# Performance work log

Measured on AMD Instinct MI355X. Metric: run time of the kernel, lower is better.

## Reference

```python
import jax, jax.numpy as jnp
import numpy as np
import math

N, T, D, H = 256, 32, 1024, 1024

def setup_inputs() -> dict:
    key = jax.random.key(0)
    k1, k2, k3, k4, k5 = jax.random.split(key, 5)
    x = jax.random.normal(k1, (N, T, D), dtype=jnp.float32)
    A = jax.random.normal(k2, (N, H, 4, 4), dtype=jnp.float32)
    Wx = jax.random.normal(k3, (D, 4 * H), dtype=jnp.float32) / math.sqrt(D)
    Wh = jax.random.normal(k4, (H, 4 * H), dtype=jnp.float32) / math.sqrt(H)
    Wattn = jax.random.normal(k5, (H, 4 * H), dtype=jnp.float32) / math.sqrt(H)
    b = jnp.zeros((4 * H,), dtype=jnp.float32)
    return {"x": x, "A": A, "Wx": Wx, "Wh": Wh, "Wattn": Wattn, "b": b}

def _forward(x, A, Wx, Wh, Wattn, b):
    Aflat = A.reshape(A.shape[0], A.shape[1], -1)  # (N, H, 16)
    h0 = Aflat.mean(axis=2)  # mean over 4x4 spatial grid -> (N, H)
    c0 = h0
    scale = 1.0 / math.sqrt(Aflat.shape[1])

    def step(carry, xt):
        prev_h, prev_c = carry
        # scaled dot-product attention over 16 spatial locations
        w = jax.nn.softmax(jnp.einsum('nh,nhl->nl', prev_h, Aflat) * scale, axis=-1)  # (N,16)
        attn = jnp.einsum('nhl,nl->nh', Aflat, w)  # (N,H)
        preact = xt @ Wx + prev_h @ Wh + attn @ Wattn + b  # (N,4H)
        ai, af, ao, ag = jnp.split(preact, 4, axis=1)
        i = jax.nn.sigmoid(ai)
        f = jax.nn.sigmoid(af)
        o = jax.nn.sigmoid(ao)
        g = jnp.tanh(ag)
        next_c = f * prev_c + i * g
        next_h = o * jnp.tanh(next_c)
        return (next_h, next_c), next_h

    xT = jnp.swapaxes(x, 0, 1)  # (T, N, D)
    _, hs = jax.lax.scan(step, (h0, c0), xT)
    return jnp.swapaxes(hs, 0, 1)  # (N, T, H)

def reference(x, A, Wx, Wh, Wattn, b):
    return _forward(x, A, Wx, Wh, Wattn, b)
```

## Files before the change

kernel.cpp:

```cpp
#include <hip/hip_runtime.h>

#define N_B 256
#define T_SEQ 32
#define DD 1024
#define HH 1024

typedef short short8 __attribute__((ext_vector_type(8)));
typedef float floatx4 __attribute__((ext_vector_type(4)));
typedef unsigned short ushort_t;

__device__ __align__(16) ushort_t g_Wxt[(size_t)4096 * 1024];
__device__ __align__(16) ushort_t g_W2 [(size_t)4096 * 2048];
__device__ __align__(16) ushort_t g_xb [(size_t)8192 * 1024];
__device__ __align__(16) float    g_px [(size_t)8192 * 4096];
__device__ __align__(16) ushort_t g_Ab [(size_t)N_B * 16384];
__device__ __align__(16) ushort_t g_At [(size_t)N_B * 16384];
__device__ __align__(16) ushort_t g_Hc[2][N_B * 2048];
__device__ __align__(16) float    g_c [N_B * HH];

__device__ __forceinline__ float bf2f(ushort_t u){
    union { unsigned int i; float f; } v; v.i = ((unsigned int)u) << 16; return v.f;
}
__device__ __forceinline__ ushort_t f2bf(float f){
    union { unsigned int i; float f; } v; v.f = f;
    unsigned int i = v.i;
    unsigned int r = (i + 0x7FFFu + ((i >> 16) & 1u)) >> 16;
    return (ushort_t)r;
}
__device__ __forceinline__ void gload16(const ushort_t* g, ushort_t* l) {
    __builtin_amdgcn_global_load_lds((const __attribute__((address_space(1))) void*)g,
                                     (__attribute__((address_space(3))) void*)l, 16, 0, 0);
}
__device__ __forceinline__ void unp8(uint4 u, float* f) {
    const ushort_t* s = (const ushort_t*)&u;
    #pragma unroll
    for (int i = 0; i < 8; ++i) f[i] = bf2f(s[i]);
}

__global__ __launch_bounds__(128) void cvt_x(const float* __restrict__ x)
{
    int b = blockIdx.x;
    int n = b >> 5, tt = b & 31;
    int tid = threadIdx.x;
    const float* src = x + (size_t)b * 1024 + tid * 8;
    float4 a = *(const float4*)src;
    float4 c = *(const float4*)(src + 4);
    ushort_t r[8];
    r[0]=f2bf(a.x); r[1]=f2bf(a.y); r[2]=f2bf(a.z); r[3]=f2bf(a.w);
    r[4]=f2bf(c.x); r[5]=f2bf(c.y); r[6]=f2bf(c.z); r[7]=f2bf(c.w);
    *(uint4*)(g_xb + (size_t)(tt * 256 + n) * 1024 + tid * 8) = *(const uint4*)r;
}

__global__ __launch_bounds__(256) void cvt_a(const float* __restrict__ A)
{
    int n = blockIdx.x, tid = threadIdx.x;
    int h0 = tid * 4;
    const float* ap = A + (size_t)n * 16384;
    ushort_t tmp[4][16];
    #pragma unroll
    for (int i = 0; i < 4; ++i) {
        const float* row = ap + (size_t)(h0 + i) * 16;
        #pragma unroll
        for (int l = 0; l < 16; ++l) tmp[i][l] = f2bf(row[l]);
        ushort_t* dst = g_Ab + (size_t)n * 16384 + (size_t)(h0 + i) * 16;
        *(uint4*)dst       = *(const uint4*)&tmp[i][0];
        *(uint4*)(dst + 8) = *(const uint4*)&tmp[i][8];
    }
    #pragma unroll
    for (int l = 0; l < 16; ++l) {
        ushort_t pk[4] = { tmp[0][l], tmp[1][l], tmp[2][l], tmp[3][l] };
        *(uint2*)(g_At + (size_t)n * 16384 + (size_t)l * 1024 + h0) = *(const uint2*)pk;
    }
}

__global__ __launch_bounds__(256) void prepack_wx(const float* __restrict__ Wx)
{
    __shared__ ushort_t tile[64][66];
    int k0 = blockIdx.x * 64, j0 = blockIdx.y * 64;
    int c = threadIdx.x & 63, r4 = threadIdx.x >> 6;
    for (int rr = 0; rr < 64; rr += 4) {
        int r = rr + r4;
        tile[r][c] = f2bf(Wx[(size_t)(k0 + r) * 4096 + j0 + c]);
    }
    __syncthreads();
    for (int rr = 0; rr < 64; rr += 4) {
        int j = rr + r4;
        g_Wxt[(size_t)(j0 + j) * 1024 + k0 + c] = tile[c][j];
    }
}

__global__ __launch_bounds__(256) void prepack_w2(
    const float* __restrict__ Wh, const float* __restrict__ Wattn)
{
    __shared__ ushort_t tile[64][66];
    int k0 = blockIdx.x * 64, j0 = blockIdx.y * 64;
    const float* src = (k0 < 1024) ? Wh : Wattn;
    int krel = (k0 < 1024) ? k0 : k0 - 1024;
    int c = threadIdx.x & 63, r4 = threadIdx.x >> 6;
    for (int rr = 0; rr < 64; rr += 4) {
        int r = rr + r4;
        tile[r][c] = f2bf(src[(size_t)(krel + r) * 4096 + j0 + c]);
    }
    __syncthreads();
    for (int rr = 0; rr < 64; rr += 4) {
        int j = rr + r4;
        g_W2[(size_t)(j0 + j) * 2048 + k0 + c] = tile[c][j];
    }
}

__global__ __launch_bounds__(256) void init_hc(const float* __restrict__ A)
{
    int gid = blockIdx.x * 256 + threadIdx.x;
    int n = gid >> 10, h = gid & 1023;
    const float* ap = A + ((size_t)gid << 4);
    float4 a0 = *(const float4*)(ap);
    float4 a1 = *(const float4*)(ap + 4);
    float4 a2 = *(const float4*)(ap + 8);
    float4 a3 = *(const float4*)(ap + 12);
    float s = (a0.x+a0.y+a0.z+a0.w) + (a1.x+a1.y+a1.z+a1.w)
            + (a2.x+a2.y+a2.z+a2.w) + (a3.x+a3.y+a3.z+a3.w);
    s *= (1.0f / 16.0f);
    g_Hc[0][n * 2048 + h] = f2bf(s);
    g_c[gid] = s;
}

__global__ __launch_bounds__(256) void xw_gemm(const float* __restrict__ bias)
{
    __shared__ __align__(16) char smem[33280];
    ushort_t* lA = (ushort_t*)smem;
    ushort_t* lB = (ushort_t*)(smem + 16384);
    float*    lP = (float*)smem;

    int b = blockIdx.x;
    int mb = b >> 5, jb = b & 31;
    int m0 = mb * 128, j0 = jb * 128;
    int tid = threadIdx.x, lane = tid & 63, wv = tid >> 6;
    int wm = wv >> 1, wn = wv & 1;
    int lm = lane & 15, quad = lane >> 4;

    int srow = lane >> 3, sseg = lane & 7;
    const ushort_t* gA = g_xb  + (size_t)(m0 + wv * 32 + srow) * 1024 + (sseg ^ srow) * 8;
    const ushort_t* gB = g_Wxt + (size_t)(j0 + wv * 32 + srow) * 1024 + (sseg ^ srow) * 8;

    floatx4 acc[4][4] = {};
    for (int kt = 0; kt < 16; ++kt) {
        __syncthreads();
        #pragma unroll
        for (int i = 0; i < 4; ++i) {
            gload16(gA + (size_t)i * 8 * 1024 + kt * 64, lA + (wv * 32 + i * 8) * 64);
            gload16(gB + (size_t)i * 8 * 1024 + kt * 64, lB + (wv * 32 + i * 8) * 64);
        }
        __syncthreads();
        #pragma unroll
        for (int ks = 0; ks < 2; ++ks) {
            short8 af[4], bf[4];
            #pragma unroll
            for (int i = 0; i < 4; ++i) {
                int row = wm*64 + i*16 + lm;
                af[i] = *(const short8*)(lA + row * 64 + (((ks*4 + quad) ^ (row & 7)) * 8));
            }
            #pragma unroll
            for (int j = 0; j < 4; ++j) {
                int row = wn*64 + j*16 + lm;
                bf[j] = *(const short8*)(lB + row * 64 + (((ks*4 + quad) ^ (row & 7)) * 8));
            }
            #pragma unroll
            for (int i = 0; i < 4; ++i)
                #pragma unroll
                for (int j = 0; j < 4; ++j)
                    acc[i][j] = __builtin_amdgcn_mfma_f32_16x16x32_bf16(af[i], bf[j], acc[i][j], 0, 0, 0);
        }
    }

    #pragma unroll
    for (int ph = 0; ph < 2; ++ph) {
        __syncthreads();
        if (wm == ph) {
            #pragma unroll
            for (int i = 0; i < 4; ++i)
                #pragma unroll
                for (int j = 0; j < 4; ++j)
                    #pragma unroll
                    for (int q = 0; q < 4; ++q)
                        lP[(i*16 + quad*4 + q) * 130 + wn*64 + j*16 + lm] = acc[i][j][q];
        }
        __syncthreads();
        int row = tid >> 2, seg = tid & 3;
        const float* src = lP + row * 130 + seg * 32;
        float* dst = g_px + (size_t)(m0 + ph * 64 + row) * 4096 + j0 + seg * 32;
        const float* bb = bias + j0 + seg * 32;
        #pragma unroll
        for (int i = 0; i < 8; ++i) {
            float4 v = *(const float4*)(src + i * 4);
            float4 w = *(const float4*)(bb + i * 4);
            v.x += w.x; v.y += w.y; v.z += w.z; v.w += w.w;
            *(float4*)(dst + i * 4) = v;
        }
    }
}

__global__ __launch_bounds__(256) void attn_step(int t)
{
    ushort_t* Hc = g_Hc[t & 1];
    int n = blockIdx.x, tid = threadIdx.x;
    int lane = tid & 63, wv = tid >> 6;
    const ushort_t* hp = Hc + n * 2048;

    int hc = lane * 16;
    float hv[16];
    unp8(*(const uint4*)(hp + hc), hv);
    unp8(*(const uint4*)(hp + hc + 8), hv + 8);

    __shared__ float red[16];
    float lg[4];
    #pragma unroll
    for (int l4 = 0; l4 < 4; ++l4) {
        int l = wv * 4 + l4;
        const ushort_t* ar = g_At + (size_t)n * 16384 + (size_t)l * 1024 + hc;
        float av[16];
        unp8(*(const uint4*)ar, av);
        unp8(*(const uint4*)(ar + 8), av + 8);
        float s = 0.f;
        #pragma unroll
        for (int i = 0; i < 16; ++i) s += hv[i] * av[i];
        s += __shfl_xor(s, 32); s += __shfl_xor(s, 16); s += __shfl_xor(s, 8);
        s += __shfl_xor(s, 4);  s += __shfl_xor(s, 2);  s += __shfl_xor(s, 1);
        lg[l4] = s;
    }
    if (lane == 0) {
        #pragma unroll
        for (int l4 = 0; l4 < 4; ++l4) red[wv * 4 + l4] = lg[l4];
    }
    __syncthreads();
    float w[16], mx = -1e30f;
    #pragma unroll
    for (int l = 0; l < 16; ++l) {
        float s = red[l] * 0.03125f;
        w[l] = s; mx = fmaxf(mx, s);
    }
    float sum = 0.f;
    #pragma unroll
    for (int l = 0; l < 16; ++l) { w[l] = __expf(w[l] - mx); sum += w[l]; }
    float inv = 1.f / sum;
    #pragma unroll
    for (int l = 0; l < 16; ++l) w[l] *= inv;

    int h0 = tid * 4;
    const ushort_t* ab = g_Ab + (size_t)n * 16384 + (size_t)h0 * 16;
    ushort_t outp[4];
    #pragma unroll
    for (int i = 0; i < 4; ++i) {
        float av[16];
        unp8(*(const uint4*)(ab + i * 16), av);
        unp8(*(const uint4*)(ab + i * 16 + 8), av + 8);
        float acc = 0.f;
        #pragma unroll
        for (int l = 0; l < 16; ++l) acc += av[l] * w[l];
        outp[i] = f2bf(acc);
    }
    *(uint2*)(Hc + n * 2048 + 1024 + h0) = *(const uint2*)outp;
}

__global__ __launch_bounds__(256, 2) void step_gemm(float* __restrict__ out, int t)
{
    __shared__ __align__(16) ushort_t lA[32 * 128];
    __shared__ __align__(16) ushort_t lB[64 * 128];
    __shared__ float lP[4][32 * 68];

    const ushort_t* Hin  = g_Hc[t & 1];
    ushort_t*       Hout = g_Hc[(t + 1) & 1];

    int b = blockIdx.x;
    int xcd = b & 7, r = b >> 3;
    int jt = xcd * 8 + (r & 7), nt = r >> 3;
    int n0 = nt * 32, hh0 = jt * 16;
    int tid = threadIdx.x, lane = tid & 63, wv = tid >> 6;
    int lm = lane & 15, quad = lane >> 4;

    int srow = lane >> 4, sseg = lane & 15;
    const ushort_t* gA0 = Hin  + (size_t)(n0 + wv * 8 + srow) * 2048;
    const ushort_t* gB0 = g_W2 + (size_t)(wv * 1024 + hh0 + srow) * 2048;

    floatx4 acc[2][4] = {};
    int segk = wv * 4 + quad;

    for (int it = 0; it < 16; ++it) {
        int kk = it * 128;
        __syncthreads();
        #pragma unroll
        for (int i = 0; i < 2; ++i) {
            int rlow = (wv * 8 + i * 4 + srow) & 15;
            gload16(gA0 + (size_t)i * 4 * 2048 + kk + (sseg ^ rlow) * 8,
                    lA + (wv * 8 + i * 4) * 128);
        }
        #pragma unroll
        for (int i = 0; i < 4; ++i) {
            int rlow = i * 4 + srow;
            gload16(gB0 + (size_t)i * 4 * 2048 + kk + (sseg ^ rlow) * 8,
                    lB + (wv * 16 + i * 4) * 128);
        }
        __syncthreads();
        short8 af[2], bf[4];
        #pragma unroll
        for (int i = 0; i < 2; ++i)
            af[i] = *(const short8*)(lA + (i * 16 + lm) * 128 + ((segk ^ lm) * 8));
        #pragma unroll
        for (int j = 0; j < 4; ++j)
            bf[j] = *(const short8*)(lB + (j * 16 + lm) * 128 + ((segk ^ lm) * 8));
        #pragma unroll
        for (int i = 0; i < 2; ++i)
            #pragma unroll
            for (int j = 0; j < 4; ++j)
                acc[i][j] = __builtin_amdgcn_mfma_f32_16x16x32_bf16(af[i], bf[j], acc[i][j], 0, 0, 0);
    }

    __syncthreads();
    float* my = &lP[wv][0];
    #pragma unroll
    for (int i = 0; i < 2; ++i)
        #pragma unroll
        for (int j = 0; j < 4; ++j)
            #pragma unroll
            for (int q = 0; q < 4; ++q)
                my[(i * 16 + quad * 4 + q) * 68 + j * 16 + lm] = acc[i][j][q];
    __syncthreads();

    #pragma unroll
    for (int e = 0; e < 2; ++e) {
        int idx = tid + e * 256;
        int nl = idx >> 4, hl = idx & 15;
        int base = nl * 68 + hl;
        float s0 = lP[0][base]      + lP[1][base]      + lP[2][base]      + lP[3][base];
        float s1 = lP[0][base + 16] + lP[1][base + 16] + lP[2][base + 16] + lP[3][base + 16];
        float s2 = lP[0][base + 32] + lP[1][base + 32] + lP[2][base + 32] + lP[3][base + 32];
        float s3 = lP[0][base + 48] + lP[1][base + 48] + lP[2][base + 48] + lP[3][base + 48];
        const float* px = g_px + ((size_t)t * 256 + (n0 + nl)) * 4096 + hh0 + hl;
        float ai  = s0 + px[0];
        float afv = s1 + px[1024];
        float ao  = s2 + px[2048];
        float ag  = s3 + px[3072];
        float iv = 1.f / (1.f + __expf(-ai));
        float fv = 1.f / (1.f + __expf(-afv));
        float ov = 1.f / (1.f + __expf(-ao));
        float gv = tanhf(ag);
        int ng = n0 + nl, hg = hh0 + hl;
        float cold = g_c[ng * 1024 + hg];
        float cnew = fv * cold + iv * gv;
        float hnew = ov * tanhf(cnew);
        g_c[ng * 1024 + hg] = cnew;
        Hout[ng * 2048 + hg] = f2bf(hnew);
        out[(size_t)ng * (T_SEQ * HH) + (size_t)t * HH + hg] = hnew;
    }
}

extern "C" void kernel_launch(void* const* d_in, const int* in_sizes, int n_in,
                              void* d_out, int out_size, void* d_ws, size_t ws_size,
                              hipStream_t stream) {
    const float* x     = (const float*)d_in[0];
    const float* A     = (const float*)d_in[1];
    const float* Wx    = (const float*)d_in[2];
    const float* Wh    = (const float*)d_in[3];
    const float* Wattn = (const float*)d_in[4];
    const float* bias  = (const float*)d_in[5];
    float* out = (float*)d_out;

    cvt_x<<<8192, 128, 0, stream>>>(x);
    cvt_a<<<256, 256, 0, stream>>>(A);
    prepack_wx<<<dim3(16, 64), 256, 0, stream>>>(Wx);
    prepack_w2<<<dim3(32, 64), 256, 0, stream>>>(Wh, Wattn);
    init_hc<<<1024, 256, 0, stream>>>(A);
    xw_gemm<<<2048, 256, 0, stream>>>(bias);
    for (int t = 0; t < T_SEQ; ++t) {
        attn_step<<<256, 256, 0, stream>>>(t);
        step_gemm<<<512, 256, 0, stream>>>(out, t);
    }
}
```

Before: 985.5 us.

## Fuse attention logits into step GEMM epilogue, double-buffer K loop, swizzle xw grid

The attention logit computation (h·A per spatial slot) moves out of attn_step into the step_gemm epilogue. Each block writes partial logits for its h-slice to g_plg, and attn_step only reduces those partials before the softmax, so the transposed A copy is no longer needed. The step_gemm K loop becomes double-buffered with explicit vmcnt waits so global-to-LDS loads overlap the MFMAs. The xw_gemm block index is remapped to group M tiles per XCD for L2 locality. Logits are now computed from fp32 h instead of bf16 h, which changes numerics slightly, and the epilogue gains extra LDS traffic and barriers.

```diff
diff --git a/kernel.cpp b/kernel.cpp
--- a/kernel.cpp
+++ b/kernel.cpp
@@ -14,9 +14,9 @@
 __device__ __align__(16) ushort_t g_xb [(size_t)8192 * 1024];
 __device__ __align__(16) float    g_px [(size_t)8192 * 4096];
 __device__ __align__(16) ushort_t g_Ab [(size_t)N_B * 16384];
-__device__ __align__(16) ushort_t g_At [(size_t)N_B * 16384];
 __device__ __align__(16) ushort_t g_Hc[2][N_B * 2048];
 __device__ __align__(16) float    g_c [N_B * HH];
+__device__ __align__(16) float    g_plg[64][N_B][16];
 
 __device__ __forceinline__ float bf2f(ushort_t u){
     union { unsigned int i; float f; } v; v.i = ((unsigned int)u) << 16; return v.f;
@@ -56,20 +56,15 @@
     int n = blockIdx.x, tid = threadIdx.x;
     int h0 = tid * 4;
     const float* ap = A + (size_t)n * 16384;
-    ushort_t tmp[4][16];
     #pragma unroll
     for (int i = 0; i < 4; ++i) {
         const float* row = ap + (size_t)(h0 + i) * 16;
-        #pragma unroll
-        for (int l = 0; l < 16; ++l) tmp[i][l] = f2bf(row[l]);
+        ushort_t tmp[16];
+        #pragma unroll
+        for (int l = 0; l < 16; ++l) tmp[l] = f2bf(row[l]);
         ushort_t* dst = g_Ab + (size_t)n * 16384 + (size_t)(h0 + i) * 16;
-        *(uint4*)dst       = *(const uint4*)&tmp[i][0];
-        *(uint4*)(dst + 8) = *(const uint4*)&tmp[i][8];
-    }
-    #pragma unroll
-    for (int l = 0; l < 16; ++l) {
-        ushort_t pk[4] = { tmp[0][l], tmp[1][l], tmp[2][l], tmp[3][l] };
-        *(uint2*)(g_At + (size_t)n * 16384 + (size_t)l * 1024 + h0) = *(const uint2*)pk;
+        *(uint4*)dst       = *(const uint4*)&tmp[0];
+        *(uint4*)(dst + 8) = *(const uint4*)&tmp[8];
     }
 }
 
@@ -110,18 +105,45 @@
 
 __global__ __launch_bounds__(256) void init_hc(const float* __restrict__ A)
 {
-    int gid = blockIdx.x * 256 + threadIdx.x;
-    int n = gid >> 10, h = gid & 1023;
+    __shared__ float l1[16 * 257];
+    __shared__ float l2[16 * 16];
+    __shared__ float lf[16];
+    int b = blockIdx.x;
+    int n = b >> 2, c = b & 3;
+    int tid = threadIdx.x;
+    int gid = b * 256 + tid;
     const float* ap = A + ((size_t)gid << 4);
-    float4 a0 = *(const float4*)(ap);
-    float4 a1 = *(const float4*)(ap + 4);
-    float4 a2 = *(const float4*)(ap + 8);
-    float4 a3 = *(const float4*)(ap + 12);
-    float s = (a0.x+a0.y+a0.z+a0.w) + (a1.x+a1.y+a1.z+a1.w)
-            + (a2.x+a2.y+a2.z+a2.w) + (a3.x+a3.y+a3.z+a3.w);
+    float a[16];
+    *(float4*)(a)      = *(const float4*)(ap);
+    *(float4*)(a + 4)  = *(const float4*)(ap + 4);
+    *(float4*)(a + 8)  = *(const float4*)(ap + 8);
+    *(float4*)(a + 12) = *(const float4*)(ap + 12);
+    float s = 0.f;
+    #pragma unroll
+    for (int l = 0; l < 16; ++l) s += a[l];
     s *= (1.0f / 16.0f);
-    g_Hc[0][n * 2048 + h] = f2bf(s);
+    g_Hc[0][n * 2048 + (c * 256 + tid)] = f2bf(s);
     g_c[gid] = s;
+    #pragma unroll
+    for (int l = 0; l < 16; ++l) l1[l * 257 + tid] = s * a[l];
+    __syncthreads();
+    {
+        int l = tid >> 4, seg = tid & 15;
+        float s2 = 0.f;
+        #pragma unroll
+        for (int i = 0; i < 16; ++i) s2 += l1[l * 257 + seg * 16 + i];
+        l2[l * 16 + seg] = s2;
+    }
+    __syncthreads();
+    if (tid < 16) {
+        float lg = 0.f;
+        #pragma unroll
+        for (int i = 0; i < 16; ++i) lg += l2[tid * 16 + i];
+        lf[tid] = lg;
+    }
+    __syncthreads();
+    int j = tid >> 4, l = tid & 15;
+    g_plg[c * 16 + j][n][l] = (j == 0) ? lf[l] : 0.f;
 }
 
 __global__ __launch_bounds__(256) void xw_gemm(const float* __restrict__ bias)
@@ -132,7 +154,8 @@
     float*    lP = (float*)smem;
 
     int b = blockIdx.x;
-    int mb = b >> 5, jb = b & 31;
+    int xcd = b & 7, q = b >> 3;
+    int mb = xcd * 8 + (q & 7), jb = q >> 3;
     int m0 = mb * 128, j0 = jb * 128;
     int tid = threadIdx.x, lane = tid & 63, wv = tid >> 6;
     int wm = wv >> 1, wn = wv & 1;
@@ -181,8 +204,8 @@
                 #pragma unroll
                 for (int j = 0; j < 4; ++j)
                     #pragma unroll
-                    for (int q = 0; q < 4; ++q)
-                        lP[(i*16 + quad*4 + q) * 130 + wn*64 + j*16 + lm] = acc[i][j][q];
+                    for (int qq = 0; qq < 4; ++qq)
+                        lP[(i*16 + quad*4 + qq) * 130 + wn*64 + j*16 + lm] = acc[i][j][qq];
         }
         __syncthreads();
         int row = tid >> 2, seg = tid & 3;
@@ -203,47 +226,39 @@
 {
     ushort_t* Hc = g_Hc[t & 1];
     int n = blockIdx.x, tid = threadIdx.x;
-    int lane = tid & 63, wv = tid >> 6;
-    const ushort_t* hp = Hc + n * 2048;
-
-    int hc = lane * 16;
-    float hv[16];
-    unp8(*(const uint4*)(hp + hc), hv);
-    unp8(*(const uint4*)(hp + hc + 8), hv + 8);
-
-    __shared__ float red[16];
-    float lg[4];
-    #pragma unroll
-    for (int l4 = 0; l4 < 4; ++l4) {
-        int l = wv * 4 + l4;
-        const ushort_t* ar = g_At + (size_t)n * 16384 + (size_t)l * 1024 + hc;
-        float av[16];
-        unp8(*(const uint4*)ar, av);
-        unp8(*(const uint4*)(ar + 8), av + 8);
+    __shared__ float redm[16 * 17];
+    __shared__ float wsh[16];
+
+    {
+        int l = tid & 15, j4 = tid >> 4;
         float s = 0.f;
         #pragma unroll
-        for (int i = 0; i < 16; ++i) s += hv[i] * av[i];
-        s += __shfl_xor(s, 32); s += __shfl_xor(s, 16); s += __shfl_xor(s, 8);
-        s += __shfl_xor(s, 4);  s += __shfl_xor(s, 2);  s += __shfl_xor(s, 1);
-        lg[l4] = s;
-    }
-    if (lane == 0) {
-        #pragma unroll
-        for (int l4 = 0; l4 < 4; ++l4) red[wv * 4 + l4] = lg[l4];
-    }
-    __syncthreads();
-    float w[16], mx = -1e30f;
-    #pragma unroll
-    for (int l = 0; l < 16; ++l) {
-        float s = red[l] * 0.03125f;
-        w[l] = s; mx = fmaxf(mx, s);
-    }
-    float sum = 0.f;
-    #pragma unroll
-    for (int l = 0; l < 16; ++l) { w[l] = __expf(w[l] - mx); sum += w[l]; }
-    float inv = 1.f / sum;
-    #pragma unroll
-    for (int l = 0; l < 16; ++l) w[l] *= inv;
+        for (int k = 0; k < 4; ++k) s += g_plg[j4 * 4 + k][n][l];
+        redm[j4 * 17 + l] = s;
+    }
+    __syncthreads();
+    if (tid < 16) {
+        float lg = 0.f;
+        #pragma unroll
+        for (int j = 0; j < 16; ++j) lg += redm[j * 17 + tid];
+        lg *= 0.03125f;
+        float mx = lg;
+        mx = fmaxf(mx, __shfl_xor(mx, 1));
+        mx = fmaxf(mx, __shfl_xor(mx, 2));
+        mx = fmaxf(mx, __shfl_xor(mx, 4));
+        mx = fmaxf(mx, __shfl_xor(mx, 8));
+        float e = __expf(lg - mx);
+        float sm = e;
+        sm += __shfl_xor(sm, 1);
+        sm += __shfl_xor(sm, 2);
+        sm += __shfl_xor(sm, 4);
+        sm += __shfl_xor(sm, 8);
+        wsh[tid] = e / sm;
+    }
+    __syncthreads();
+    float w[16];
+    #pragma unroll
+    for (int i = 0; i < 16; ++i) w[i] = wsh[i];
 
     int h0 = tid * 4;
     const ushort_t* ab = g_Ab + (size_t)n * 16384 + (size_t)h0 * 16;
@@ -263,9 +278,13 @@
 
 __global__ __launch_bounds__(256, 2) void step_gemm(float* __restrict__ out, int t)
 {
-    __shared__ __align__(16) ushort_t lA[32 * 128];
-    __shared__ __align__(16) ushort_t lB[64 * 128];
-    __shared__ float lP[4][32 * 68];
+    __shared__ __align__(16) char smem[49152];
+    ushort_t* lA0 = (ushort_t*)smem;
+    ushort_t* lA1 = (ushort_t*)(smem + 8192);
+    ushort_t* lB0 = (ushort_t*)(smem + 16384);
+    ushort_t* lB1 = (ushort_t*)(smem + 32768);
+    float*    lP  = (float*)smem;
+    float*    lq  = (float*)smem;
 
     const ushort_t* Hin  = g_Hc[t & 1];
     ushort_t*       Hout = g_Hc[(t + 1) & 1];
@@ -284,38 +303,58 @@
     floatx4 acc[2][4] = {};
     int segk = wv * 4 + quad;
 
+    #pragma unroll
+    for (int i = 0; i < 2; ++i) {
+        int rlow = (wv * 8 + i * 4 + srow) & 15;
+        gload16(gA0 + (size_t)i * 4 * 2048 + (sseg ^ rlow) * 8, lA0 + (wv * 8 + i * 4) * 128);
+    }
+    #pragma unroll
+    for (int i = 0; i < 4; ++i) {
+        int rlow = i * 4 + srow;
+        gload16(gB0 + (size_t)i * 4 * 2048 + (sseg ^ rlow) * 8, lB0 + (wv * 16 + i * 4) * 128);
+    }
+
     for (int it = 0; it < 16; ++it) {
-        int kk = it * 128;
-        __syncthreads();
-        #pragma unroll
-        for (int i = 0; i < 2; ++i) {
-            int rlow = (wv * 8 + i * 4 + srow) & 15;
-            gload16(gA0 + (size_t)i * 4 * 2048 + kk + (sseg ^ rlow) * 8,
-                    lA + (wv * 8 + i * 4) * 128);
-        }
-        #pragma unroll
-        for (int i = 0; i < 4; ++i) {
-            int rlow = i * 4 + srow;
-            gload16(gB0 + (size_t)i * 4 * 2048 + kk + (sseg ^ rlow) * 8,
-                    lB + (wv * 16 + i * 4) * 128);
-        }
-        __syncthreads();
-        short8 af[2], bf[4];
+        ushort_t* cA = (it & 1) ? lA1 : lA0;
+        ushort_t* cB = (it & 1) ? lB1 : lB0;
+        ushort_t* nA = (it & 1) ? lA0 : lA1;
+        ushort_t* nB = (it & 1) ? lB0 : lB1;
+        if (it < 15) {
+            int kk = (it + 1) * 128;
+            #pragma unroll
+            for (int i = 0; i < 2; ++i) {
+                int rlow = (wv * 8 + i * 4 + srow) & 15;
+                gload16(gA0 + (size_t)i * 4 * 2048 + kk + (sseg ^ rlow) * 8,
+                        nA + (wv * 8 + i * 4) * 128);
+            }
+            #pragma unroll
+            for (int i = 0; i < 4; ++i) {
+                int rlow = i * 4 + srow;
+                gload16(gB0 + (size_t)i * 4 * 2048 + kk + (sseg ^ rlow) * 8,
+                        nB + (wv * 16 + i * 4) * 128);
+            }
+            asm volatile("s_waitcnt vmcnt(6)" ::: "memory");
+        } else {
+            asm volatile("s_waitcnt vmcnt(0)" ::: "memory");
+        }
+        __builtin_amdgcn_s_barrier();
+        short8 af[2], bq[4];
         #pragma unroll
         for (int i = 0; i < 2; ++i)
-            af[i] = *(const short8*)(lA + (i * 16 + lm) * 128 + ((segk ^ lm) * 8));
+            af[i] = *(const short8*)(cA + (i * 16 + lm) * 128 + ((segk ^ lm) * 8));
         #pragma unroll
         for (int j = 0; j < 4; ++j)
-            bf[j] = *(const short8*)(lB + (j * 16 + lm) * 128 + ((segk ^ lm) * 8));
+            bq[j] = *(const short8*)(cB + (j * 16 + lm) * 128 + ((segk ^ lm) * 8));
         #pragma unroll
         for (int i = 0; i < 2; ++i)
             #pragma unroll
             for (int j = 0; j < 4; ++j)
-                acc[i][j] = __builtin_amdgcn_mfma_f32_16x16x32_bf16(af[i], bf[j], acc[i][j], 0, 0, 0);
-    }
-
-    __syncthreads();
-    float* my = &lP[wv][0];
+                acc[i][j] = __builtin_amdgcn_mfma_f32_16x16x32_bf16(af[i], bq[j], acc[i][j], 0, 0, 0);
+        asm volatile("s_waitcnt lgkmcnt(0)" ::: "memory");
+        __builtin_amdgcn_s_barrier();
+    }
+
+    float* my = lP + wv * (32 * 68);
     #pragma unroll
     for (int i = 0; i < 2; ++i)
         #pragma unroll
@@ -325,15 +364,16 @@
                 my[(i * 16 + quad * 4 + q) * 68 + j * 16 + lm] = acc[i][j][q];
     __syncthreads();
 
+    float hsave[2];
     #pragma unroll
     for (int e = 0; e < 2; ++e) {
         int idx = tid + e * 256;
         int nl = idx >> 4, hl = idx & 15;
         int base = nl * 68 + hl;
-        float s0 = lP[0][base]      + lP[1][base]      + lP[2][base]      + lP[3][base];
-        float s1 = lP[0][base + 16] + lP[1][base + 16] + lP[2][base + 16] + lP[3][base + 16];
-        float s2 = lP[0][base + 32] + lP[1][base + 32] + lP[2][base + 32] + lP[3][base + 32];
-        float s3 = lP[0][base + 48] + lP[1][base + 48] + lP[2][base + 48] + lP[3][base + 48];
+        float s0 = lP[base]      + lP[2176 + base]      + lP[4352 + base]      + lP[6528 + base];
+        float s1 = lP[base + 16] + lP[2176 + base + 16] + lP[4352 + base + 16] + lP[6528 + base + 16];
+        float s2 = lP[base + 32] + lP[2176 + base + 32] + lP[4352 + base + 32] + lP[6528 + base + 32];
+        float s3 = lP[base + 48] + lP[2176 + base + 48] + lP[4352 + base + 48] + lP[6528 + base + 48];
         const float* px = g_px + ((size_t)t * 256 + (n0 + nl)) * 4096 + hh0 + hl;
         float ai  = s0 + px[0];
         float afv = s1 + px[1024];
@@ -350,6 +390,34 @@
         g_c[ng * 1024 + hg] = cnew;
         Hout[ng * 2048 + hg] = f2bf(hnew);
         out[(size_t)ng * (T_SEQ * HH) + (size_t)t * HH + hg] = hnew;
+        hsave[e] = hnew;
+    }
+
+    if (t < 31) {
+        __syncthreads();
+        #pragma unroll
+        for (int e = 0; e < 2; ++e) {
+            int idx = tid + e * 256;
+            int nl = idx >> 4, hl = idx & 15;
+            const ushort_t* ar = g_Ab + (size_t)(n0 + nl) * 16384 + (size_t)(hh0 + hl) * 16;
+            float av[16];
+            unp8(*(const uint4*)ar, av);
+            unp8(*(const uint4*)(ar + 8), av + 8);
+            float hv = hsave[e];
+            #pragma unroll
+            for (int l = 0; l < 16; ++l)
+                lq[(nl * 16 + l) * 17 + hl] = hv * av[l];
+        }
+        __syncthreads();
+        #pragma unroll
+        for (int e = 0; e < 2; ++e) {
+            int idx = tid + e * 256;
+            int nl = idx >> 4, l = idx & 15;
+            float s = 0.f;
+            #pragma unroll
+            for (int k = 0; k < 16; ++k) s += lq[(nl * 16 + l) * 17 + k];
+            g_plg[jt][n0 + nl][l] = s;
+        }
     }
 }
 
```

Measured after the change: 948.8 us. -3.7%, faster.
